# Kernel optimization log

Measured on AMD Instinct MI355X. Metric: run time of the kernel, lower is better.

The kernel has to match this reference:

```python
import jax, jax.numpy as jnp
import numpy as np

BS, C, H, W = 128, 256, 9, 9
D = 9                      # spectral window size
PS = 15                    # padsize
PAD_SPACE = PS - H         # 6
PAD1 = D // 2              # 4 (spectral pad)
START = PAD_SPACE // 2     # 3 (output crop offset)
SPE_HEAD = 25
SHARE_HEAD = 9
SIDE = 5                   # spe_head_Sidelength
BN_EPS = 1e-5


def setup_inputs() -> dict:
    key = jax.random.key(0)
    ks = jax.random.split(key, 12)
    s = 0.1
    return {
        "x": jax.random.normal(ks[0], (BS, C, H, W), jnp.float32),
        "wk": jax.random.normal(ks[1], (H * W, 1, D), jnp.float32) * s,   # depthwise conv1d over spectral axis
        "bk": jax.random.normal(ks[2], (H * W,), jnp.float32) * s,
        "w1": jax.random.normal(ks[3], (SPE_HEAD, SHARE_HEAD, 2 * SHARE_HEAD), jnp.float32) * s,  # grouped 1x1, no bias
        "bn_gamma": jnp.ones((SPE_HEAD * SHARE_HEAD,), jnp.float32),
        "bn_beta": jnp.zeros((SPE_HEAD * SHARE_HEAD,), jnp.float32),
        "bn_mean": jax.random.normal(ks[4], (SPE_HEAD * SHARE_HEAD,), jnp.float32) * s,
        "bn_var": jax.random.uniform(ks[5], (SPE_HEAD * SHARE_HEAD,), jnp.float32, 0.5, 1.5),
        "w2": jax.random.normal(ks[6], (SPE_HEAD, D, SHARE_HEAD), jnp.float32) * s,  # grouped 1x1 -> spe_head*d
        "b2": jax.random.normal(ks[7], (SPE_HEAD * D,), jnp.float32) * s,
        "wv": jax.random.normal(ks[8], (C, 1, 3, 3), jnp.float32) * s,   # depthwise 3x3
        "bv": jax.random.normal(ks[9], (C,), jnp.float32) * s,
    }


def _unfold_k3_d5(t, bs, c):
    # torch nn.Unfold(kernel=3, dilation=5) on a 15x15 map -> 5x5 output positions.
    # row = kh*5 + oh, col = kw*5 + ow, so a plain (3,5,3,5) reshape gives the taps.
    t = t.reshape(bs, c, 3, SIDE, 3, SIDE)              # (bs,c,kh,oh,kw,ow)
    t = t.transpose(0, 1, 2, 4, 3, 5)                   # (bs,c,kh,kw,oh,ow)
    t = t.reshape(bs, c * SHARE_HEAD, SPE_HEAD)          # (bs, c*9, 25) torch unfold layout
    return t.transpose(0, 2, 1)                          # (bs, 25, c*9)


def reference(x, wk, bk, w1, bn_gamma, bn_beta, bn_mean, bn_var, w2, b2, wv, bv):
    bs, c, h, w = x.shape
    # --- key: depthwise conv1d along spectral (channel) axis, one filter per pixel ---
    k = x.reshape(bs, c, h * w).transpose(0, 2, 1)       # (bs, 81, c)
    k1 = jax.lax.conv_general_dilated(
        k, wk, (1,), [(PAD1, PAD1)],
        dimension_numbers=("NCH", "OIH", "NCH"), feature_group_count=h * w,
    ) + bk[None, :, None]                                # (bs, 81, c)
    k1 = k1.transpose(0, 2, 1).reshape(bs, c, h, w)

    # --- pad right/bottom and unfold q, k ---
    k1_pad = jnp.pad(k1, ((0, 0), (0, 0), (0, PAD_SPACE), (0, PAD_SPACE)))  # (bs,c,15,15)
    q_pad = jnp.pad(x, ((0, 0), (0, 0), (0, PAD_SPACE), (0, PAD_SPACE)))
    key_u = _unfold_k3_d5(k1_pad, bs, c)                 # (bs,25,9c)
    q_u = _unfold_k3_d5(q_pad, bs, c)

    # stack + reshape exactly as torch (row-major): (bs,25,2,9c) -> (bs,450,c)
    key_q = jnp.stack((q_u, key_u), axis=2).reshape(bs, 2 * SPE_HEAD * SHARE_HEAD, c)

    # --- attention_embed: grouped 1x1 conv -> BN(eval) -> ReLU -> grouped 1x1 conv ---
    a = jnp.einsum("goi,bgic->bgoc", w1, key_q.reshape(bs, SPE_HEAD, 2 * SHARE_HEAD, c))
    a = a.reshape(bs, SPE_HEAD * SHARE_HEAD, c)          # (bs,225,c)
    inv_std = bn_gamma / jnp.sqrt(bn_var + BN_EPS)
    a = (a - bn_mean[None, :, None]) * inv_std[None, :, None] + bn_beta[None, :, None]
    a = jax.nn.relu(a)
    a = jnp.einsum("goi,bgic->bgoc", w2, a.reshape(bs, SPE_HEAD, SHARE_HEAD, c))
    a = a.reshape(bs, SPE_HEAD * D, c) + b2[None, :, None]  # (bs,225,c)

    # --- build per-pixel spectral kernels: tile, rearrange to 15x15, softmax over d ---
    att = jnp.tile(a.reshape(bs, SPE_HEAD, D, c), (1, SHARE_HEAD, 1, 1))  # (bs,225,9,c)
    att = att.transpose(0, 3, 1, 2)                      # (bs,c,225,d)
    att = att.reshape(bs, c, 3, 3, SIDE, SIDE, D)
    att = att.transpose(0, 1, 2, 4, 3, 5, 6)             # swap dims 3,4 as torch .transpose(3,4)
    att = att.reshape(bs, c, PS, PS, D)
    att = jax.nn.softmax(att, axis=-1)
    att = att.transpose(0, 1, 4, 2, 3)                   # (bs,c,d,15,15)

    # --- value: depthwise 3x3 conv, pad left/top + spectral, sliding window over channels ---
    v = jax.lax.conv_general_dilated(
        x, wv, (1, 1), [(1, 1), (1, 1)],
        dimension_numbers=("NCHW", "OIHW", "NCHW"), feature_group_count=c,
    ) + bv[None, :, None, None]                          # (bs,c,9,9)
    pv = jnp.pad(v, ((0, 0), (PAD1, PAD1), (PAD_SPACE, 0), (PAD_SPACE, 0)))  # (bs,c+8,15,15)
    v_unf = jnp.stack([pv[:, t:t + c] for t in range(D)], axis=2)            # (bs,c,d,15,15)

    out = jnp.sum(v_unf * att, axis=2) + k1_pad          # (bs,c,15,15)
    return out[:, :, START:h + START, START:w + START]    # (bs,c,9,9)
```

## Files before the change

### kernel.cpp

```cpp
#include <hip/hip_runtime.h>

#define C 256
#define HW 81
#define PITCH 292
#define PITCHD 146
#define ZROW 81

typedef __fp16 h2 __attribute__((ext_vector_type(2)));

__device__ __forceinline__ float us2f(unsigned short u) {
  union { unsigned short s; __fp16 h; } c; c.s = u; return (float)c.h;
}
__device__ __forceinline__ float lo_h(unsigned int d) {
  union { unsigned int i; h2 h; } c; c.i = d; return (float)c.h.x;
}
__device__ __forceinline__ float hi_h(unsigned int d) {
  union { unsigned int i; h2 h; } c; c.i = d; return (float)c.h.y;
}
__device__ __forceinline__ unsigned int pkh2(float a, float b) {
  union { h2 h; unsigned int i; } c;
  c.h = __builtin_amdgcn_cvt_pkrtz(a, b);
  return c.i;
}
__device__ __forceinline__ h2 as_h2(unsigned int d) {
  union { unsigned int i; h2 h; } c; c.i = d; return c.h;
}
__device__ __forceinline__ unsigned int as_u32(h2 h) {
  union { h2 h; unsigned int i; } c; c.h = h; return c.i;
}
__device__ __forceinline__ float dot2(unsigned int a, unsigned int b, float c) {
#if __has_builtin(__builtin_amdgcn_fdot2)
  return __builtin_amdgcn_fdot2(as_h2(a), as_h2(b), c, false);
#else
  h2 x = as_h2(a), y = as_h2(b);
  return fmaf((float)x.y, (float)y.y, fmaf((float)x.x, (float)y.x, c));
#endif
}
__device__ __forceinline__ float exp2_fast(float x) {
#if __has_builtin(__builtin_amdgcn_exp2f)
  return __builtin_amdgcn_exp2f(x);
#else
  return __expf(x * 0.6931471805599453f);
#endif
}

__global__ __launch_bounds__(1024) void semca_fused(
    const float* __restrict__ x, const float* __restrict__ wk,
    const float* __restrict__ bk, const float* __restrict__ w1,
    const float* __restrict__ gamma, const float* __restrict__ beta,
    const float* __restrict__ mean, const float* __restrict__ var,
    const float* __restrict__ w2, const float* __restrict__ b2,
    const float* __restrict__ wv, const float* __restrict__ bv,
    float* __restrict__ out) {
  __shared__ unsigned short xT[82 * PITCH];
  __shared__ unsigned short k1T[82 * PITCH];
  __shared__ unsigned short vT[18 * PITCH];
  __shared__ unsigned short pixtab[228];
  __shared__ float bnf1[225];
  __shared__ unsigned int w1p[225 * 12];
  __shared__ unsigned int w2p[225 * 4];
  __shared__ uint2 wkp[81 * 3];

  const int blk = blockIdx.x;
  const int b = (blk & 7) * 16 + ((blk >> 3) & 15);
  const int s = blk >> 7;
  const int tid = threadIdx.x;
  const float* xb = x + (size_t)b * (C * HW);

  unsigned int* xTd = (unsigned int*)xT;
  unsigned int* k1Td = (unsigned int*)k1T;
  unsigned int* vTd = (unsigned int*)vT;
  unsigned int* wkpd = (unsigned int*)wkp;

  float xe[11], xo[11];
  int adr[11];
  {
    int chp = tid / HW;
    int p = tid - chp * HW;
#pragma unroll
    for (int rep = 0; rep < 10; ++rep) {
      const float* base = xb + (2 * chp) * HW + p;
      xe[rep] = base[0];
      xo[rep] = base[HW];
      adr[rep] = PITCHD * p + 2 + chp;
      chp += 12;
      p += 52;
      if (p >= HW) { p -= HW; chp += 1; }
    }
    if (tid < 128) {
      int f = 10240 + tid;
      int c2 = f / HW, p2 = f - c2 * HW;
      xe[10] = xb[2 * c2 * HW + p2];
      xo[10] = xb[(2 * c2 + 1) * HW + p2];
      adr[10] = PITCHD * p2 + 2 + c2;
    }
  }

  for (int t = tid; t < 810; t += 1024) {
    int p = t / 10, k2 = t - (t / 10) * 10;
    xT[p * PITCH + ((k2 < 4) ? k2 : (256 + k2))] = 0;
  }
  if (tid < PITCHD) {
    xTd[PITCHD * ZROW + tid] = 0;
    k1Td[PITCHD * ZROW + tid] = 0;
  }
  for (int t = tid; t < 225; t += 1024) {
    int g = t / 9, tap = t - (t / 9) * 9;
    int kh = tap / 3, kw = tap - kh * 3;
    int h = kh * 5 + g / 5, w = kw * 5 + (g - (g / 5) * 5);
    pixtab[t] = (h < 9 && w < 9) ? (unsigned short)((h * 9 + w) * PITCH)
                                 : (unsigned short)(ZROW * PITCH);
    float inv = gamma[t] * rsqrtf(var[t] + 1e-5f);
    bnf1[t] = beta[t] - mean[t] * inv;
  }
  for (int t = tid; t < 2025; t += 1024) {
    int m = t / 9, q = t - m * 9;
    float inv = gamma[m] * rsqrtf(var[m] + 1e-5f);
    w1p[m * 12 + q] = pkh2(w1[m * 18 + q] * inv, w1[m * 18 + 9 + q] * inv);
  }
  if (tid < 900) {
    int m = tid >> 2, j = tid & 3;
    w2p[m * 4 + j] = pkh2(w2[m * 9 + 2 * j], w2[m * 9 + 2 * j + 1]);
  }
  if (tid < 486) {
    int m = tid / 6, j = tid - (tid / 6) * 6;
    const float* wr = wk + m * 9;
    unsigned int v;
    if (j < 4)       v = pkh2(wr[2 * j], wr[2 * j + 1]);
    else if (j == 4) v = pkh2(wr[8], 0.f);
    else             v = pkh2(0.f, wr[8]);
    wkpd[m * 6 + j] = v;
  }

  const int chv = tid & 127;
  unsigned int wvp[9];
#pragma unroll
  for (int t = 0; t < 9; ++t)
    wvp[t] = pkh2(wv[(2 * chv) * 9 + t], wv[(2 * chv + 1) * 9 + t]);
  const unsigned int bvp = pkh2(bv[2 * chv], bv[2 * chv + 1]);

#pragma unroll
  for (int rep = 0; rep < 10; ++rep) xTd[adr[rep]] = pkh2(xe[rep], xo[rep]);
  if (tid < 128) xTd[adr[10]] = pkh2(xe[10], xo[10]);

  __syncthreads();

  {
    auto k1fn8 = [&](int p, int oct) {
      const uint2* wrow2 = (const uint2*)(xTd + PITCHD * p + 4 * oct);
      uint2 r0 = wrow2[0], r1 = wrow2[1], r2 = wrow2[2], r3 = wrow2[3];
      unsigned int W[8] = {r0.x, r0.y, r1.x, r1.y, r2.x, r2.y, r3.x, r3.y};
      unsigned int A[7];
#pragma unroll
      for (int k2 = 0; k2 < 7; ++k2)
        A[k2] = (W[k2] >> 16) | (W[k2 + 1] << 16);
      const uint2* wkq = wkp + p * 3;
      uint2 wa = wkq[0], wb = wkq[1], wc = wkq[2];
      float bkp = bk[p];
      float cc[8];
#pragma unroll
      for (int j2 = 0; j2 < 4; ++j2) {
        cc[2 * j2] =
            dot2(W[j2], wa.x, dot2(W[j2 + 1], wa.y, dot2(W[j2 + 2], wb.x,
            dot2(W[j2 + 3], wb.y, dot2(W[j2 + 4], wc.x, bkp)))));
        cc[2 * j2 + 1] =
            dot2(A[j2], wa.x, dot2(A[j2 + 1], wa.y, dot2(A[j2 + 2], wb.x,
            dot2(A[j2 + 3], wb.y, dot2(W[j2 + 4], wc.y, bkp)))));
      }
      unsigned int* dst = k1Td + PITCHD * p + 2 + 4 * oct;
      *(uint2*)dst = make_uint2(pkh2(cc[0], cc[1]), pkh2(cc[2], cc[3]));
      *(uint2*)(dst + 2) = make_uint2(pkh2(cc[4], cc[5]), pkh2(cc[6], cc[7]));
    };
    auto prow = [&](int f) {
      int idx = f >> 5;
      int ri = idx / 9, col = idx - ri * 9;
      int row = s == 0 ? (ri + ((ri < 3) ? 1 : 3)) : (ri + ((ri >= 2) ? 1 : 0));
      return row * 9 + col;
    };
    k1fn8(prow(tid), tid & 31);
    if (tid < 704) {
      int f = 1024 + tid;
      k1fn8(prow(f), f & 31);
    }
  }

  {
    auto vfn = [&](int f) {
      int e = __builtin_amdgcn_readfirstlane(f >> 7);
      int r0 = e / 6;
      int i = s * 3 + r0;
      int j = e - r0 * 6;
      h2 acc = as_h2(bvp);
#pragma unroll
      for (int di = 0; di < 3; ++di) {
        int ii = i + di - 1;
        if (ii < 0) continue;
#pragma unroll
        for (int dj = 0; dj < 3; ++dj) {
          int jj = j + dj - 1;
          if (jj < 0) continue;
          unsigned int d = xTd[PITCHD * (ii * 9 + jj) + 2 + chv];
          int t = di * 3 + dj;
          acc = as_h2(d) * as_h2(wvp[t]) + acc;
        }
      }
      vTd[PITCHD * e + 2 + chv] = as_u32(acc);
    };
#pragma unroll
    for (int rep = 0; rep < 2; ++rep) vfn(tid + rep * 1024);
    if (tid < 256) vfn(2048 + tid);
  }
  if (tid < 180) {
    int e = tid / 10, k2 = tid - (tid / 10) * 10;
    vT[e * PITCH + ((k2 < 4) ? k2 : (256 + k2))] = 0;
  }
  __syncthreads();

  const int s4 = tid >> 8;
  const int ch = tid & 255;
  const int ci0 = ch / 9;
  const int tap0 = ch - ci0 * 9;
  float* outb = out + ((size_t)b * C + ch) * HW;

  int tq[9], cq[9];
  {
    int ci = ci0, tap = tap0;
#pragma unroll
    for (int q = 0; q < 9; ++q) {
      tq[q] = tap;
      cq[q] = 4 + ci;
      tap += 4;
      ci += 28;
      if (tap >= 9) { tap -= 9; ci += 1; }
    }
  }

#define PV_STORE(OH, OW)                                                   \
  do {                                                                     \
    int e_ = gh_i * 6 + ((OW)-3);                                          \
    const unsigned short* vrow_ = vT + e_ * PITCH;                         \
    float acc_ = 0.f;                                                      \
    _Pragma("unroll") for (int d_ = 0; d_ < 9; ++d_) acc_ =                \
        fmaf(a2[d_], us2f(vrow_[ch + d_]), acc_);                          \
    if ((OH) < 6 && (OW) < 6)                                              \
      acc_ = fmaf(acc_, inv_s,                                             \
                  us2f(k1T[(((OH) + 3) * 9 + ((OW) + 3)) * PITCH + 4 + ch])); \
    else                                                                   \
      acc_ *= inv_s;                                                       \
    outb[(OH)*9 + (OW)] = acc_;                                            \
  } while (0)

#pragma unroll
  for (int k = 0; k < 4; ++k) {
    if (s4 == 3 && k == 3) break;
    int idx = s4 * 4 + k;
    int gh_i = idx / 5, gw_i = idx - (idx / 5) * 5;
    int oh = (s ? 6 : 3) + gh_i;
    int gh = s ? ((gh_i + 4) % 5) : (gh_i + 1);
    int g9 = __builtin_amdgcn_readfirstlane((gh * 5 + gw_i) * 9);

    unsigned int kqp[9];
#pragma unroll
    for (int q = 0; q < 9; ++q) {
      int off = (int)pixtab[g9 + tq[q]] + cq[q];
      unsigned int xv = xT[off], kv = k1T[off];
      kqp[q] = xv | (kv << 16);
    }

    __builtin_amdgcn_s_setprio(1);
    float r[9];
#pragma unroll
    for (int o = 0; o < 9; ++o) {
      int m = g9 + o;
      const unsigned int* wp = w1p + m * 12;
      float a = bnf1[m];
#pragma unroll
      for (int q = 0; q < 9; ++q) a = dot2(kqp[q], wp[q], a);
      r[o] = fmaxf(a, 0.f);
    }

    unsigned int rp[4];
#pragma unroll
    for (int j = 0; j < 4; ++j) rp[j] = pkh2(r[2 * j], r[2 * j + 1]);
    float a2[9], mx = -1e30f;
#pragma unroll
    for (int d = 0; d < 9; ++d) {
      int m = g9 + d;
      const unsigned int* wq = w2p + m * 4;
      float a = b2[m];
#pragma unroll
      for (int j = 0; j < 4; ++j) a = dot2(rp[j], wq[j], a);
      a = fmaf(w2[m * 9 + 8], r[8], a);
      a2[d] = a;
      mx = fmaxf(mx, a);
    }
    const float L2E = 1.44269504f;
    float nmL = mx * -L2E;
    float ssum = 0.f;
#pragma unroll
    for (int d = 0; d < 9; ++d) {
      a2[d] = exp2_fast(fmaf(a2[d], L2E, nmL));
      ssum += a2[d];
    }
    float inv_s = __builtin_amdgcn_rcpf(ssum);
    __builtin_amdgcn_s_setprio(0);

    int ow0 = (gw_i == 0) ? 7 : (gw_i + 2);
    PV_STORE(oh, ow0);
    if (gw_i == 1) PV_STORE(oh, 8);
  }
#undef PV_STORE

  if (s == 0) {
    if (s4 == 3) {
#pragma unroll
      for (int r0 = 0; r0 < 3; ++r0) {
        int oh = 3 + r0;
#pragma unroll
        for (int ow = 0; ow < 3; ++ow)
          outb[oh * 9 + ow] =
              us2f(k1T[((oh + 3) * 9 + (ow + 3)) * PITCH + 4 + ch]);
      }
    }
  } else {
    if (s4 < 3) {
      int oh = s4;
#pragma unroll
      for (int ow = 0; ow < 9; ++ow) {
        float v2 = 0.f;
        if (ow < 6)
          v2 = us2f(k1T[((oh + 3) * 9 + (ow + 3)) * PITCH + 4 + ch]);
        outb[oh * 9 + ow] = v2;
      }
    } else {
#pragma unroll
      for (int r0 = 0; r0 < 3; ++r0) {
        int oh = 6 + r0;
        outb[oh * 9 + 0] = 0.f;
        outb[oh * 9 + 1] = 0.f;
        outb[oh * 9 + 2] = 0.f;
      }
    }
  }
}

extern "C" void kernel_launch(void* const* d_in, const int* in_sizes, int n_in,
                              void* d_out, int out_size, void* d_ws, size_t ws_size,
                              hipStream_t stream) {
  const float* x     = (const float*)d_in[0];
  const float* wk    = (const float*)d_in[1];
  const float* bk    = (const float*)d_in[2];
  const float* w1    = (const float*)d_in[3];
  const float* gamma = (const float*)d_in[4];
  const float* beta  = (const float*)d_in[5];
  const float* mean  = (const float*)d_in[6];
  const float* var   = (const float*)d_in[7];
  const float* w2    = (const float*)d_in[8];
  const float* b2    = (const float*)d_in[9];
  const float* wv    = (const float*)d_in[10];
  const float* bv    = (const float*)d_in[11];
  float* out = (float*)d_out;

  hipLaunchKernelGGL(semca_fused, dim3(256), dim3(1024), 0, stream,
                     x, wk, bk, w1, gamma, beta, mean, var, w2, b2, wv, bv, out);
}
```

Baseline: 24.39 us.

## Use packed fp16 dot2 for value aggregation via shifted duplicate value buffer

Adds a second value buffer shifted by one fp16 element, so every channel can read its 9-tap window as dword-aligned fp16 pairs. The softmax weights are packed into half2 and aggregated with 5 fdot2 ops instead of 9 scalar fp16 loads and FMAs. The w2 projection is extended to 5 packed words, which removes the scalar tail FMA. The s==1 edge-store work is moved so that the s4==3 threads handle it instead of s4<3. This costs extra LDS, an extra store during the value build, and fp16 rounding of the attention weights.

```diff
diff --git a/kernel.cpp b/kernel.cpp
--- a/kernel.cpp
+++ b/kernel.cpp
@@ -10,12 +10,6 @@
 
 __device__ __forceinline__ float us2f(unsigned short u) {
   union { unsigned short s; __fp16 h; } c; c.s = u; return (float)c.h;
-}
-__device__ __forceinline__ float lo_h(unsigned int d) {
-  union { unsigned int i; h2 h; } c; c.i = d; return (float)c.h.x;
-}
-__device__ __forceinline__ float hi_h(unsigned int d) {
-  union { unsigned int i; h2 h; } c; c.i = d; return (float)c.h.y;
 }
 __device__ __forceinline__ unsigned int pkh2(float a, float b) {
   union { h2 h; unsigned int i; } c;
@@ -55,10 +49,11 @@
   __shared__ unsigned short xT[82 * PITCH];
   __shared__ unsigned short k1T[82 * PITCH];
   __shared__ unsigned short vT[18 * PITCH];
+  __shared__ unsigned short vT2[18 * PITCH];
   __shared__ unsigned short pixtab[228];
   __shared__ float bnf1[225];
   __shared__ unsigned int w1p[225 * 12];
-  __shared__ unsigned int w2p[225 * 4];
+  __shared__ unsigned int w2p[225 * 5];
   __shared__ uint2 wkp[81 * 3];
 
   const int blk = blockIdx.x;
@@ -118,9 +113,10 @@
     float inv = gamma[m] * rsqrtf(var[m] + 1e-5f);
     w1p[m * 12 + q] = pkh2(w1[m * 18 + q] * inv, w1[m * 18 + 9 + q] * inv);
   }
-  if (tid < 900) {
-    int m = tid >> 2, j = tid & 3;
-    w2p[m * 4 + j] = pkh2(w2[m * 9 + 2 * j], w2[m * 9 + 2 * j + 1]);
+  for (int t = tid; t < 1125; t += 1024) {
+    int m = t / 5, j = t - (t / 5) * 5;
+    w2p[t] = (j < 4) ? pkh2(w2[m * 9 + 2 * j], w2[m * 9 + 2 * j + 1])
+                     : pkh2(w2[m * 9 + 8], 0.f);
   }
   if (tid < 486) {
     int m = tid / 6, j = tid - (tid / 6) * 6;
@@ -204,15 +200,24 @@
           acc = as_h2(d) * as_h2(wvp[t]) + acc;
         }
       }
-      vTd[PITCHD * e + 2 + chv] = as_u32(acc);
+      unsigned int u = as_u32(acc);
+      vTd[PITCHD * e + 2 + chv] = u;
+      vT2[PITCH * e + 3 + 2 * chv] = (unsigned short)(u & 0xffffu);
+      vT2[PITCH * e + 4 + 2 * chv] = (unsigned short)(u >> 16);
     };
 #pragma unroll
     for (int rep = 0; rep < 2; ++rep) vfn(tid + rep * 1024);
     if (tid < 256) vfn(2048 + tid);
   }
-  if (tid < 180) {
-    int e = tid / 10, k2 = tid - (tid / 10) * 10;
-    vT[e * PITCH + ((k2 < 4) ? k2 : (256 + k2))] = 0;
+  if (tid < 432) {
+    if (tid < 216) {
+      int e = tid / 12, k2 = tid - (tid / 12) * 12;
+      vT[e * PITCH + ((k2 < 4) ? k2 : (256 + k2))] = 0;
+    } else {
+      int t2 = tid - 216;
+      int e = t2 / 12, k2 = t2 - (t2 / 12) * 12;
+      vT2[e * PITCH + ((k2 < 3) ? k2 : (256 + k2))] = 0;
+    }
   }
   __syncthreads();
 
@@ -221,6 +226,10 @@
   const int ci0 = ch / 9;
   const int tap0 = ch - ci0 * 9;
   float* outb = out + ((size_t)b * C + ch) * HW;
+
+  const unsigned int* pvrow =
+      ((ch & 1) ? (const unsigned int*)vT2 : (const unsigned int*)vT) +
+      (ch >> 1);
 
   int tq[9], cq[9];
   {
@@ -238,10 +247,10 @@
 #define PV_STORE(OH, OW)                                                   \
   do {                                                                     \
     int e_ = gh_i * 6 + ((OW)-3);                                          \
-    const unsigned short* vrow_ = vT + e_ * PITCH;                         \
+    const unsigned int* vp_ = pvrow + e_ * PITCHD;                         \
     float acc_ = 0.f;                                                      \
-    _Pragma("unroll") for (int d_ = 0; d_ < 9; ++d_) acc_ =                \
-        fmaf(a2[d_], us2f(vrow_[ch + d_]), acc_);                          \
+    _Pragma("unroll") for (int j_ = 0; j_ < 5; ++j_) acc_ =                \
+        dot2(vp_[j_], ap[j_], acc_);                                       \
     if ((OH) < 6 && (OW) < 6)                                              \
       acc_ = fmaf(acc_, inv_s,                                             \
                   us2f(k1T[(((OH) + 3) * 9 + ((OW) + 3)) * PITCH + 4 + ch])); \
@@ -279,18 +288,18 @@
       r[o] = fmaxf(a, 0.f);
     }
 
-    unsigned int rp[4];
+    unsigned int rp[5];
 #pragma unroll
     for (int j = 0; j < 4; ++j) rp[j] = pkh2(r[2 * j], r[2 * j + 1]);
+    rp[4] = pkh2(r[8], 0.f);
     float a2[9], mx = -1e30f;
 #pragma unroll
     for (int d = 0; d < 9; ++d) {
       int m = g9 + d;
-      const unsigned int* wq = w2p + m * 4;
+      const unsigned int* wq = w2p + m * 5;
       float a = b2[m];
 #pragma unroll
-      for (int j = 0; j < 4; ++j) a = dot2(rp[j], wq[j], a);
-      a = fmaf(w2[m * 9 + 8], r[8], a);
+      for (int j = 0; j < 5; ++j) a = dot2(rp[j], wq[j], a);
       a2[d] = a;
       mx = fmaxf(mx, a);
     }
@@ -303,6 +312,10 @@
       ssum += a2[d];
     }
     float inv_s = __builtin_amdgcn_rcpf(ssum);
+    unsigned int ap[5];
+#pragma unroll
+    for (int j = 0; j < 4; ++j) ap[j] = pkh2(a2[2 * j], a2[2 * j + 1]);
+    ap[4] = pkh2(a2[8], 0.f);
     __builtin_amdgcn_s_setprio(0);
 
     int ow0 = (gw_i == 0) ? 7 : (gw_i + 2);
@@ -311,8 +324,8 @@
   }
 #undef PV_STORE
 
-  if (s == 0) {
-    if (s4 == 3) {
+  if (s4 == 3) {
+    if (s == 0) {
 #pragma unroll
       for (int r0 = 0; r0 < 3; ++r0) {
         int oh = 3 + r0;
@@ -321,18 +334,18 @@
           outb[oh * 9 + ow] =
               us2f(k1T[((oh + 3) * 9 + (ow + 3)) * PITCH + 4 + ch]);
       }
-    }
-  } else {
-    if (s4 < 3) {
-      int oh = s4;
-#pragma unroll
-      for (int ow = 0; ow < 9; ++ow) {
-        float v2 = 0.f;
-        if (ow < 6)
-          v2 = us2f(k1T[((oh + 3) * 9 + (ow + 3)) * PITCH + 4 + ch]);
-        outb[oh * 9 + ow] = v2;
-      }
     } else {
+#pragma unroll
+      for (int r0 = 0; r0 < 3; ++r0) {
+        int oh = r0;
+#pragma unroll
+        for (int ow = 0; ow < 9; ++ow) {
+          float v2 = 0.f;
+          if (ow < 6)
+            v2 = us2f(k1T[((oh + 3) * 9 + (ow + 3)) * PITCH + 4 + ch]);
+          outb[oh * 9 + ow] = v2;
+        }
+      }
 #pragma unroll
       for (int r0 = 0; r0 < 3; ++r0) {
         int oh = 6 + r0;
```

After: 25.88 us. 1.06x slower.
